# Kernel optimization log

Measured on AMD Instinct MI355X. Metric: run time of the kernel, lower is better.

## Reference

```python
import jax, jax.numpy as jnp
import numpy as np

D, N, M = 256, 8192, 8192
DISTANCE_THRESH = 0.8


def setup_inputs() -> dict:
    key = jax.random.key(0)
    k0, k1 = jax.random.split(key)
    d0 = jax.random.normal(k0, (D, N), dtype=jnp.float32)
    d1 = jax.random.normal(k1, (D, M), dtype=jnp.float32)
    # descriptors are L2-normalized along the feature dim (cosine similarity,
    # consistent with the 2*(1-sim) squared-distance formula in the module)
    d0 = d0 / jnp.linalg.norm(d0, axis=0, keepdims=True)
    d1 = d1 / jnp.linalg.norm(d1, axis=0, keepdims=True)
    return {"descriptors0": d0, "descriptors1": d1}


def reference(descriptors0, descriptors1):
    # nn_sim: [N, M] similarity matrix
    nn_sim = jnp.einsum('dn,dm->nm', descriptors0, descriptors1)
    nn_dist_01 = jnp.max(nn_sim, axis=1)          # [N]
    nn_idx_01 = jnp.argmax(nn_sim, axis=1)        # [N]
    nn_idx_10 = jnp.argmax(nn_sim, axis=0)        # [M]
    nn_dist = 2.0 * (1.0 - nn_dist_01)            # squared L2 dist for unit vecs
    ids1 = jnp.arange(nn_sim.shape[0])
    mask = ids1 == nn_idx_10[nn_idx_01]           # mutual NN check
    if DISTANCE_THRESH > 0.0:
        mask = mask & (nn_dist <= DISTANCE_THRESH ** 2)
    matches = jnp.where(mask, nn_idx_01, -1)
    scores = jnp.where(mask, (nn_dist + 1.0) / 2.0, 0.0)
    return matches, scores
```

## Files before the change

kernel.cpp:

```cpp
#include <hip/hip_runtime.h>
#include <hip/hip_bf16.h>

typedef __attribute__((ext_vector_type(8))) short short8;
typedef __attribute__((ext_vector_type(4))) float floatx4;
typedef unsigned int u32;

#define D_DIM 256
#define TCOLS 32
#define TILES 16
#define IDX_BITS 0x1FFFu
#define VAL_MASK 0xFFFFE000u


__device__ inline unsigned short f2bf_rne(float f) {
  u32 u = __float_as_uint(f);
  u32 r = (u + 0x7FFFu + ((u >> 16) & 1u)) >> 16;
  return (unsigned short)r;
}

__device__ inline u32 umax(u32 a, u32 b) { return a > b ? a : b; }

__device__ inline void async_ld16(const void* g, void* l) {
  __builtin_amdgcn_global_load_lds((const __attribute__((address_space(1))) void*)g,
                                   (__attribute__((address_space(3))) void*)l, 16, 0, 0);
}


__global__ __launch_bounds__(256) void transpose_cast(const float* __restrict__ src,
                                                      unsigned short* __restrict__ dst, int C,
                                                      u32* __restrict__ best, int init_n) {
  const int tid = threadIdx.x;
  const int d = blockIdx.x * 64 + (tid & 63);
  const int chunk = blockIdx.y * 4 + (tid >> 6);
  const int f0 = chunk * 8;
  float v[8];
#pragma unroll
  for (int u = 0; u < 8; ++u) v[u] = src[(size_t)(f0 + u) * C + d];
  short8 o;
#pragma unroll
  for (int u = 0; u < 8; ++u) o[u] = (short)f2bf_rne(v[u]);
  *(short8*)(dst + (size_t)d * D_DIM + f0) = o;
  if (blockIdx.y == 0) {
    int i = blockIdx.x * 256 + tid;
    if (i < init_n) best[i] = 0u;
  }
}

__global__ __launch_bounds__(256, 1) void gemm_reduce(const float* __restrict__ A,
                                                      const unsigned short* __restrict__ Bt,
                                                      u32* __restrict__ best01,
                                                      u32* __restrict__ best10,
                                                      int N) {
  __shared__ alignas(16) unsigned short sB[2][TCOLS * D_DIM];

  const int tid  = threadIdx.x;
  const int wave = tid >> 6;
  const int lane = tid & 63;
  const int quad = lane >> 4;
  const int l15  = lane & 15;
  const int n0   = blockIdx.x * 256;
  const int mg0  = blockIdx.y * (TILES * TCOLS);
  const int rbase = n0 + wave * 64;

  {
    const unsigned short* src = Bt + (size_t)mg0 * D_DIM;
#pragma unroll
    for (int c = 0; c < 4; ++c) {
      int slot = c * 256 + tid;
      int r = slot >> 5, cc = slot & 31;
      int ccg = (cc & 24) | ((cc ^ r) & 7);
      async_ld16(src + (size_t)r * D_DIM + ccg * 8, (unsigned short*)sB[0] + slot * 8);
    }
  }

  short8 af[4][8];
#pragma unroll
  for (int t = 0; t < 4; ++t)
#pragma unroll
    for (int kc = 0; kc < 8; ++kc) {
      const int row = rbase + t * 16 + l15;
      const int kb = kc * 32 + quad * 8;
      short8 o;
#pragma unroll
      for (int u = 0; u < 8; ++u)
        o[u] = (short)f2bf_rne(A[(size_t)(kb + u) * N + row]);
      af[t][kc] = o;
    }

  u32 rbk[16];
#pragma unroll
  for (int s = 0; s < 16; ++s) rbk[s] = 0u;

  __syncthreads();

  for (int mt = 0; mt < TILES; ++mt) {
    const int m0 = mg0 + mt * TCOLS;
    if (mt + 1 < TILES) {
      const unsigned short* src = Bt + (size_t)(m0 + TCOLS) * D_DIM;
      unsigned short* dstb = (unsigned short*)sB[(mt + 1) & 1];
#pragma unroll
      for (int c = 0; c < 4; ++c) {
        int slot = c * 256 + tid;
        int r = slot >> 5, cc = slot & 31;
        int ccg = (cc & 24) | ((cc ^ r) & 7);
        async_ld16(src + (size_t)r * D_DIM + ccg * 8, dstb + slot * 8);
      }
    }

    floatx4 acc[4][2];
#pragma unroll
    for (int i = 0; i < 4; ++i)
#pragma unroll
      for (int j = 0; j < 2; ++j)
        acc[i][j] = (floatx4){2.0f, 2.0f, 2.0f, 2.0f};

    const unsigned short* sb = (const unsigned short*)sB[mt & 1];
#pragma unroll
    for (int kc = 0; kc < 8; ++kc) {
      short8 bfr[2];
#pragma unroll
      for (int j = 0; j < 2; ++j) {
        int c2 = j * 16 + l15;
        int ch = kc * 4 + quad;
        int chg = (ch & 24) | ((ch ^ c2) & 7);
        bfr[j] = *(const short8*)(sb + c2 * D_DIM + chg * 8);
      }
#pragma unroll
      for (int i = 0; i < 4; ++i)
#pragma unroll
        for (int j = 0; j < 2; ++j)
          acc[i][j] = __builtin_amdgcn_mfma_f32_16x16x32_bf16(af[i][kc], bfr[j], acc[i][j], 0, 0, 0);
    }

    u32 cb[2] = {0u, 0u};
    u32 colpay[2];
#pragma unroll
    for (int j = 0; j < 2; ++j) colpay[j] = (~(u32)(m0 + j * 16 + l15)) & IDX_BITS;
#pragma unroll
    for (int i = 0; i < 4; ++i)
#pragma unroll
      for (int r = 0; r < 4; ++r) {
        u32 rowpay = (~(u32)(rbase + i * 16 + quad * 4 + r)) & IDX_BITS;
        u32 rb = rbk[i * 4 + r];
#pragma unroll
        for (int j = 0; j < 2; ++j) {
          u32 u = __float_as_uint(acc[i][j][r]) & VAL_MASK;
          rb = umax(rb, u | colpay[j]);
          cb[j] = umax(cb[j], u | rowpay);
        }
        rbk[i * 4 + r] = rb;
      }
#pragma unroll
    for (int j = 0; j < 2; ++j) {
      u32 b = cb[j];
      b = umax(b, (u32)__shfl_xor((int)b, 16, 64));
      b = umax(b, (u32)__shfl_xor((int)b, 32, 64));
      if (quad == 0) atomicMax(&best10[m0 + j * 16 + l15], b);
    }
    __syncthreads();
  }

#pragma unroll
  for (int i = 0; i < 4; ++i)
#pragma unroll
    for (int r = 0; r < 4; ++r) {
      u32 b = rbk[i * 4 + r];
      b = umax(b, (u32)__shfl_xor((int)b, 1, 64));
      b = umax(b, (u32)__shfl_xor((int)b, 2, 64));
      b = umax(b, (u32)__shfl_xor((int)b, 4, 64));
      b = umax(b, (u32)__shfl_xor((int)b, 8, 64));
      if (l15 == 0) atomicMax(&best01[rbase + i * 16 + quad * 4 + r], b);
    }
}

__global__ void finalize(const u32* __restrict__ best01, const u32* __restrict__ best10,
                         float* __restrict__ out, int N) {
  int n = blockIdx.x * blockDim.x + threadIdx.x;
  if (n >= N) return;
  u32 k = best01[n];
  int idx01 = (int)((~k) & IDX_BITS);
  float sim = __uint_as_float(k & VAL_MASK) - 2.0f;
  int idx10 = (int)((~best10[idx01]) & IDX_BITS);
  float dist = 2.0f - 2.0f * sim;
  bool ok = (idx10 == n) && (dist <= 0.64f);
  out[n]     = ok ? (float)idx01 : -1.0f;
  out[N + n] = ok ? 1.5f - sim : 0.0f;
}


extern "C" void kernel_launch(void* const* d_in, const int* in_sizes, int n_in,
                              void* d_out, int out_size, void* d_ws, size_t ws_size,
                              hipStream_t stream) {
  (void)n_in; (void)out_size; (void)ws_size;
  const float* d0 = (const float*)d_in[0];
  const float* d1 = (const float*)d_in[1];
  const int N = in_sizes[0] / D_DIM;
  const int M = in_sizes[1] / D_DIM;

  u32* best01 = (u32*)d_ws;
  u32* best10 = best01 + N;
  unsigned short* Bt = (unsigned short*)(best10 + M);
  float* out = (float*)d_out;

  hipLaunchKernelGGL(transpose_cast, dim3(M / 64, 8), dim3(256), 0, stream,
                     d1, Bt, M, best01, N + M);
  hipLaunchKernelGGL(gemm_reduce, dim3(N / 256, M / (TILES * TCOLS)), dim3(256), 0, stream,
                     d0, Bt, best01, best10, N);
  hipLaunchKernelGGL(finalize, dim3(N / 256), dim3(256), 0, stream, best01, best10, out, N);
}
```

Before: 104.4 us.

## Precast A to bf16 row-major, halve M tiles, and buffer column maxima in LDS

Adds a separate transpose_cast pass that converts descriptors0 into a bf16 row-major buffer when workspace allows, so the GEMM loads A fragments with vector loads instead of strided fp32 gathers plus per-element conversion. It also halves TILES, giving twice as many blocks, and raises the launch-bounds occupancy hint to 4 blocks per CU. Per-tile column maxima now go to shared-memory atomics and are flushed to global once per block, which cuts global atomic traffic. Costs are an extra kernel launch, extra workspace, and A fragments being reloaded by more blocks.

```diff
diff --git a/kernel.cpp b/kernel.cpp
--- a/kernel.cpp
+++ b/kernel.cpp
@@ -7,7 +7,7 @@
 
 #define D_DIM 256
 #define TCOLS 32
-#define TILES 16
+#define TILES 8
 #define IDX_BITS 0x1FFFu
 #define VAL_MASK 0xFFFFE000u
 
@@ -46,12 +46,15 @@
   }
 }
 
-__global__ __launch_bounds__(256, 1) void gemm_reduce(const float* __restrict__ A,
+template <bool PRECAST>
+__global__ __launch_bounds__(256, 4) void gemm_reduce(const float* __restrict__ A,
+                                                      const unsigned short* __restrict__ At,
                                                       const unsigned short* __restrict__ Bt,
                                                       u32* __restrict__ best01,
                                                       u32* __restrict__ best10,
                                                       int N) {
   __shared__ alignas(16) unsigned short sB[2][TCOLS * D_DIM];
+  __shared__ u32 colbest[TILES * TCOLS];
 
   const int tid  = threadIdx.x;
   const int wave = tid >> 6;
@@ -62,6 +65,8 @@
   const int mg0  = blockIdx.y * (TILES * TCOLS);
   const int rbase = n0 + wave * 64;
 
+  colbest[tid] = 0u;
+
   {
     const unsigned short* src = Bt + (size_t)mg0 * D_DIM;
 #pragma unroll
@@ -74,22 +79,38 @@
   }
 
   short8 af[4][8];
-#pragma unroll
-  for (int t = 0; t < 4; ++t)
-#pragma unroll
-    for (int kc = 0; kc < 8; ++kc) {
-      const int row = rbase + t * 16 + l15;
-      const int kb = kc * 32 + quad * 8;
-      short8 o;
-#pragma unroll
-      for (int u = 0; u < 8; ++u)
-        o[u] = (short)f2bf_rne(A[(size_t)(kb + u) * N + row]);
-      af[t][kc] = o;
-    }
+  if constexpr (PRECAST) {
+#pragma unroll
+    for (int t = 0; t < 4; ++t) {
+      const unsigned short* ap = At + (size_t)(rbase + t * 16 + l15) * D_DIM + quad * 8;
+#pragma unroll
+      for (int kc = 0; kc < 8; ++kc)
+        af[t][kc] = *(const short8*)(ap + kc * 32);
+    }
+  } else {
+#pragma unroll
+    for (int t = 0; t < 4; ++t)
+#pragma unroll
+      for (int kc = 0; kc < 8; ++kc) {
+        const int row = rbase + t * 16 + l15;
+        const int kb = kc * 32 + quad * 8;
+        short8 o;
+#pragma unroll
+        for (int u = 0; u < 8; ++u)
+          o[u] = (short)f2bf_rne(A[(size_t)(kb + u) * N + row]);
+        af[t][kc] = o;
+      }
+  }
 
   u32 rbk[16];
-#pragma unroll
-  for (int s = 0; s < 16; ++s) rbk[s] = 0u;
+  u32 rowpay[16];
+#pragma unroll
+  for (int i = 0; i < 4; ++i)
+#pragma unroll
+    for (int r = 0; r < 4; ++r) {
+      rbk[i * 4 + r] = 0u;
+      rowpay[i * 4 + r] = (~(u32)(rbase + i * 16 + quad * 4 + r)) & IDX_BITS;
+    }
 
   __syncthreads();
 
@@ -140,13 +161,13 @@
     for (int i = 0; i < 4; ++i)
 #pragma unroll
       for (int r = 0; r < 4; ++r) {
-        u32 rowpay = (~(u32)(rbase + i * 16 + quad * 4 + r)) & IDX_BITS;
+        u32 rp = rowpay[i * 4 + r];
         u32 rb = rbk[i * 4 + r];
 #pragma unroll
         for (int j = 0; j < 2; ++j) {
           u32 u = __float_as_uint(acc[i][j][r]) & VAL_MASK;
           rb = umax(rb, u | colpay[j]);
-          cb[j] = umax(cb[j], u | rowpay);
+          cb[j] = umax(cb[j], u | rp);
         }
         rbk[i * 4 + r] = rb;
       }
@@ -155,7 +176,7 @@
       u32 b = cb[j];
       b = umax(b, (u32)__shfl_xor((int)b, 16, 64));
       b = umax(b, (u32)__shfl_xor((int)b, 32, 64));
-      if (quad == 0) atomicMax(&best10[m0 + j * 16 + l15], b);
+      if (quad == 0) atomicMax(&colbest[mt * TCOLS + j * 16 + l15], b);
     }
     __syncthreads();
   }
@@ -171,6 +192,8 @@
       b = umax(b, (u32)__shfl_xor((int)b, 8, 64));
       if (l15 == 0) atomicMax(&best01[rbase + i * 16 + quad * 4 + r], b);
     }
+
+  atomicMax(&best10[mg0 + tid], colbest[tid]);
 }
 
 __global__ void finalize(const u32* __restrict__ best01, const u32* __restrict__ best10,
@@ -191,7 +214,7 @@
 extern "C" void kernel_launch(void* const* d_in, const int* in_sizes, int n_in,
                               void* d_out, int out_size, void* d_ws, size_t ws_size,
                               hipStream_t stream) {
-  (void)n_in; (void)out_size; (void)ws_size;
+  (void)n_in; (void)out_size;
   const float* d0 = (const float*)d_in[0];
   const float* d1 = (const float*)d_in[1];
   const int N = in_sizes[0] / D_DIM;
@@ -199,12 +222,26 @@
 
   u32* best01 = (u32*)d_ws;
   u32* best10 = best01 + N;
-  unsigned short* Bt = (unsigned short*)(best10 + M);
+  unsigned short* At = (unsigned short*)(best10 + M);
+  unsigned short* Bt = At + (size_t)N * D_DIM;
   float* out = (float*)d_out;
 
-  hipLaunchKernelGGL(transpose_cast, dim3(M / 64, 8), dim3(256), 0, stream,
-                     d1, Bt, M, best01, N + M);
-  hipLaunchKernelGGL(gemm_reduce, dim3(N / 256, M / (TILES * TCOLS)), dim3(256), 0, stream,
-                     d0, Bt, best01, best10, N);
+  const size_t need = (size_t)(N + M) * sizeof(u32) +
+                      (size_t)(N + M) * D_DIM * sizeof(unsigned short);
+
+  if (ws_size >= need) {
+    hipLaunchKernelGGL(transpose_cast, dim3(N / 64, 8), dim3(256), 0, stream,
+                       d0, At, N, best01, N + M);
+    hipLaunchKernelGGL(transpose_cast, dim3(M / 64, 8), dim3(256), 0, stream,
+                       d1, Bt, M, best01, 0);
+    hipLaunchKernelGGL((gemm_reduce<true>), dim3(N / 256, M / (TILES * TCOLS)), dim3(256),
+                       0, stream, d0, At, Bt, best01, best10, N);
+  } else {
+    unsigned short* BtF = (unsigned short*)(best10 + M);
+    hipLaunchKernelGGL(transpose_cast, dim3(M / 64, 8), dim3(256), 0, stream,
+                       d1, BtF, M, best01, N + M);
+    hipLaunchKernelGGL((gemm_reduce<false>), dim3(N / 256, M / (TILES * TCOLS)), dim3(256),
+                       0, stream, d0, BtF, BtF, best01, best10, N);
+  }
   hipLaunchKernelGGL(finalize, dim3(N / 256), dim3(256), 0, stream, best01, best10, out, N);
 }
```

Measured after the change: 258.1 us. +147.3%, slower.
